# Performance work log

Hardware: AMD Instinct MI355X
Metric: run time of the kernel (lower is better)

## Reference

```python
import jax, jax.numpy as jnp
import numpy as np

E = 64      # ENTITY_EMBED_DIM
NH = 4      # ATTN_NUM_HEADS
HD = E // NH
H = 128     # RNN_HIDDEN_SIZE
LN_EPS = 1e-5

def _leaky(x):
    return jnp.where(x >= 0, x, 0.01 * x)

def setup_inputs() -> dict:
    key = jax.random.key(0)
    ks = jax.random.split(key, 20)
    def n(k, shape, s=0.1):
        return (jax.random.normal(k, shape, jnp.float32) * s)
    B, S = 128, 1024
    return {
        'obs': jax.random.normal(ks[0], (B, S, 12), jnp.float32),
        'hidden_state': jnp.zeros((1, B, H), jnp.float32),
        # missile encoder: Linear(3,32) -> LeakyReLU -> Linear(32,64)
        'me_w1': n(ks[1], (32, 3)), 'me_b1': jnp.zeros((32,), jnp.float32),
        'me_w2': n(ks[2], (64, 32)), 'me_b2': jnp.zeros((64,), jnp.float32),
        # aircraft encoder: Linear(6,32) -> LeakyReLU -> Linear(32,64)
        'ae_w1': n(ks[3], (32, 6)), 'ae_b1': jnp.zeros((32,), jnp.float32),
        'ae_w2': n(ks[4], (64, 32)), 'ae_b2': jnp.zeros((64,), jnp.float32),
        # MultiheadAttention packed in_proj (q,k,v) + out_proj
        'in_proj_w': n(ks[5], (3 * E, E)), 'in_proj_b': jnp.zeros((3 * E,), jnp.float32),
        'out_proj_w': n(ks[6], (E, E)), 'out_proj_b': jnp.zeros((E,), jnp.float32),
        # LayerNorm
        'ln_g': jnp.ones((E,), jnp.float32), 'ln_b': jnp.zeros((E,), jnp.float32),
        # GRU (r,z,n gate order, torch convention)
        'gru_w_ih': n(ks[7], (3 * H, E)), 'gru_w_hh': n(ks[8], (3 * H, H)),
        'gru_b_ih': jnp.zeros((3 * H,), jnp.float32), 'gru_b_hh': jnp.zeros((3 * H,), jnp.float32),
        # post-GRU MLP: Linear(128,128)+LeakyReLU x2
        'mlp_w0': n(ks[9], (128, 128)), 'mlp_b0': jnp.zeros((128,), jnp.float32),
        'mlp_w1': n(ks[10], (128, 128)), 'mlp_b1': jnp.zeros((128,), jnp.float32),
        # value head
        'out_w': n(ks[11], (1, 128)), 'out_b': jnp.zeros((1,), jnp.float32),
    }

def reference(obs, hidden_state, me_w1, me_b1, me_w2, me_b2, ae_w1, ae_b1, ae_w2, ae_b2,
              in_proj_w, in_proj_b, out_proj_w, out_proj_b, ln_g, ln_b,
              gru_w_ih, gru_w_hh, gru_b_ih, gru_b_hh,
              mlp_w0, mlp_b0, mlp_w1, mlp_b1, out_w, out_b):
    B, S, _ = obs.shape
    m1 = obs[..., 0:3]
    m2 = obs[..., 3:6]
    ac = obs[..., 6:12]

    def enc(x, w1, b1, w2, b2):
        return _leaky(x @ w1.T + b1) @ w2.T + b2

    m1e = enc(m1, me_w1, me_b1, me_w2, me_b2)   # [B,S,E]
    m2e = enc(m2, me_w1, me_b1, me_w2, me_b2)   # [B,S,E]
    ace = enc(ac, ae_w1, ae_b1, ae_w2, ae_b2)   # [B,S,E]

    # Cross-attention: 1 query (aircraft), 2 keys/values (missiles) per (b,s)
    wq, wk, wv = in_proj_w[:E], in_proj_w[E:2 * E], in_proj_w[2 * E:]
    bq, bk, bv = in_proj_b[:E], in_proj_b[E:2 * E], in_proj_b[2 * E:]
    q = ace @ wq.T + bq                          # [B,S,E]
    kv_in = jnp.stack([m1e, m2e], axis=2)        # [B,S,2,E]
    k = kv_in @ wk.T + bk                        # [B,S,2,E]
    v = kv_in @ wv.T + bv
    qh = q.reshape(B, S, NH, HD)
    kh = k.reshape(B, S, 2, NH, HD)
    vh = v.reshape(B, S, 2, NH, HD)
    scale = 1.0 / np.sqrt(HD)
    scores = jnp.einsum('bshd,bsnhd->bshn', qh, kh) * scale  # [B,S,NH,2]
    attn = jax.nn.softmax(scores, axis=-1)
    ctx = jnp.einsum('bshn,bsnhd->bshd', attn, vh).reshape(B, S, E)
    attn_out = ctx @ out_proj_w.T + out_proj_b

    # residual + LayerNorm
    x = attn_out + ace
    mu = jnp.mean(x, axis=-1, keepdims=True)
    var = jnp.mean((x - mu) ** 2, axis=-1, keepdims=True)
    xn = (x - mu) * jax.lax.rsqrt(var + LN_EPS) * ln_g + ln_b  # [B,S,E]

    # GRU over S (torch gate order r,z,n)
    xp = xn @ gru_w_ih.T + gru_b_ih  # [B,S,3H]

    def step(h, xt):
        hp = h @ gru_w_hh.T + gru_b_hh
        xr, xz, xg = jnp.split(xt, 3, axis=-1)
        hr, hz, hg = jnp.split(hp, 3, axis=-1)
        r = jax.nn.sigmoid(xr + hr)
        z = jax.nn.sigmoid(xz + hz)
        g = jnp.tanh(xg + r * hg)
        h_new = (1.0 - z) * g + z * h
        return h_new, h_new

    h_last, outs = jax.lax.scan(step, hidden_state[0], jnp.swapaxes(xp, 0, 1))
    gru_out = jnp.swapaxes(outs, 0, 1)  # [B,S,H]

    f = _leaky(gru_out @ mlp_w0.T + mlp_b0)
    f = _leaky(f @ mlp_w1.T + mlp_b1)
    value = f @ out_w.T + out_b  # [B,S,1]
    return value, h_last[None]
```

## Files before the change

kernel.cpp:

```cpp
#include <hip/hip_runtime.h>
#include <hip/hip_bf16.h>

#define BB 128
#define SS 1024
#define HH 128
#define G3 384
#define NT (BB * SS)

typedef __hip_bfloat16 bf16;
typedef unsigned int uint;
typedef unsigned short ushort;
typedef _Float16 f16;
typedef f16 f16x2 __attribute__((ext_vector_type(2)));
typedef f16 f16x8 __attribute__((ext_vector_type(8)));
typedef float f32x4 __attribute__((ext_vector_type(4)));

__device__ __forceinline__ float leaky(float x) { return x >= 0.f ? x : 0.01f * x; }
__device__ __forceinline__ f16x2 u2h(uint u) { return __builtin_bit_cast(f16x2, u); }
__device__ __forceinline__ uint packh2(float a, float b) {
  f16x2 h; h.x = (f16)a; h.y = (f16)b;
  return __builtin_bit_cast(uint, h);
}
__device__ __forceinline__ uint h1(float a) {
  return (uint)__builtin_bit_cast(ushort, (f16)a);
}
__device__ __forceinline__ uint bf_rne(float f) {
  uint u = __float_as_uint(f);
  return (u + 0x7FFFu + ((u >> 16) & 1u)) >> 16;
}
__device__ __forceinline__ float shflx(float v, int m) { return __shfl_xor(v, m, 64); }
__device__ __forceinline__ float dpp_xor1(float v) {
  int i = __builtin_bit_cast(int, v);
  i = __builtin_amdgcn_update_dpp(0, i, 0xB1, 0xF, 0xF, true);
  return __builtin_bit_cast(float, i);
}
__device__ __forceinline__ uint dpp_xor1_u(uint v) {
  int i = __builtin_amdgcn_update_dpp(0, (int)v, 0xB1, 0xF, 0xF, true);
  return (uint)i;
}
#define WSYNC() asm volatile("s_waitcnt lgkmcnt(0)" ::: "memory")

template <int NP>
__device__ __forceinline__ void ldrow(const float* __restrict__ p, f16x2* w) {
#pragma unroll
  for (int i = 0; i < NP; ++i) {
    f16x2 h; h.x = (f16)p[2 * i]; h.y = (f16)p[2 * i + 1];
    w[i] = h;
  }
}
__device__ __forceinline__ f16x8 ldw8(const float* __restrict__ p) {
  f16x8 v;
#pragma unroll
  for (int j = 0; j < 8; ++j) v[j] = (f16)p[j];
  return v;
}
template <int NP>
__device__ __forceinline__ float dot2l(const uint* __restrict__ x,
                                       const f16x2* __restrict__ w, float acc) {
#pragma unroll
  for (int i = 0; i < NP / 4; ++i) {
    uint4 uu = ((const uint4*)x)[i];
    acc = __builtin_amdgcn_fdot2(u2h(uu.x), w[4 * i + 0], acc, false);
    acc = __builtin_amdgcn_fdot2(u2h(uu.y), w[4 * i + 1], acc, false);
    acc = __builtin_amdgcn_fdot2(u2h(uu.z), w[4 * i + 2], acc, false);
    acc = __builtin_amdgcn_fdot2(u2h(uu.w), w[4 * i + 3], acc, false);
  }
  return acc;
}
__device__ __forceinline__ float d4(uint4 x, uint4 w, float acc) {
  acc = __builtin_amdgcn_fdot2(u2h(x.x), u2h(w.x), acc, false);
  acc = __builtin_amdgcn_fdot2(u2h(x.y), u2h(w.y), acc, false);
  acc = __builtin_amdgcn_fdot2(u2h(x.z), u2h(w.z), acc, false);
  acc = __builtin_amdgcn_fdot2(u2h(x.w), u2h(w.w), acc, false);
  return acc;
}

__global__ __launch_bounds__(256, 4) void pre_a(
    const float* __restrict__ obs, const float* __restrict__ me_w1,
    const float* __restrict__ me_b1, const float* __restrict__ me_w2,
    const float* __restrict__ me_b2, const float* __restrict__ ae_w1,
    const float* __restrict__ ae_b1, const float* __restrict__ ae_w2,
    const float* __restrict__ ae_b2, const float* __restrict__ ipw,
    const float* __restrict__ ipb, const float* __restrict__ opw,
    const float* __restrict__ opb, const float* __restrict__ lng,
    const float* __restrict__ lnb, uint* __restrict__ xnh) {
  __shared__ float ss[352];
  __shared__ __align__(16) uint4 w4[8 * 256];
  __shared__ __align__(16) uint ex[4][176];

  const int tid = threadIdx.x;
  const int wid = tid >> 6, l = tid & 63;
  if (tid < 96) ss[tid] = me_w1[tid];
  if (tid < 32) ss[96 + tid] = me_b1[tid];
  if (tid < 192) ss[128 + tid] = ae_w1[tid];
  if (tid < 32) ss[320 + tid] = ae_b1[tid];

  for (int idx = tid; idx < 2048; idx += 256) {
    const int r = idx & 255, c = idx >> 8;
    const float* src =
        (r < 192 ? ipw + (size_t)r * 64 : opw + (size_t)(r - 192) * 64) + c * 8;
    uint4 u;
    u.x = packh2(src[0], src[1]);
    u.y = packh2(src[2], src[3]);
    u.z = packh2(src[4], src[5]);
    u.w = packh2(src[6], src[7]);
    w4[(c << 8) + r] = u;
  }

  f16x2 wme2[16], wae2[16];
  ldrow<16>(me_w2 + l * 32, wme2);
  ldrow<16>(ae_w2 + l * 32, wae2);
  const float bme2 = me_b2[l], bae2 = ae_b2[l];
  const float bq = ipb[l], bk = ipb[64 + l], bv = ipb[128 + l], bop = opb[l];
  const float gl = lng[l], bl = lnb[l];
  __syncthreads();

  uint* um = ex[wid];
  uint* ua = um + 32;
  uint* e1 = um + 48;
  uint* e2 = um + 80;
  uint* ea = um + 112;
  uint* ec = um + 144;

  for (int base = blockIdx.x * 4; base < NT; base += 4096) {
    const size_t token = base + wid;
    const float4* ob4 = (const float4*)(obs + token * 12);
    float4 o0 = ob4[0], o1 = ob4[1], o2 = ob4[2];

    const int row = l & 31;
    const bool m2h = l >= 32;
    float i0 = m2h ? o0.w : o0.x, i1 = m2h ? o1.x : o0.y, i2 = m2h ? o1.y : o0.z;
    float t1 = ss[96 + row] + i0 * ss[row * 3] + i1 * ss[row * 3 + 1] + i2 * ss[row * 3 + 2];
    t1 = leaky(t1);
    float ta = ss[320 + row] + o1.z * ss[128 + row * 6] + o1.w * ss[128 + row * 6 + 1] +
               o2.x * ss[128 + row * 6 + 2] + o2.y * ss[128 + row * 6 + 3] +
               o2.z * ss[128 + row * 6 + 4] + o2.w * ss[128 + row * 6 + 5];
    ta = leaky(ta);
    float t1p = shflx(t1, 1), tap = shflx(ta, 1);
    if (!(l & 1)) {
      um[l >> 1] = packh2(t1, t1p);
      if (l < 32) ua[l >> 1] = packh2(ta, tap);
    }
    WSYNC();

    float m1e = dot2l<16>(um, wme2, bme2);
    float m2e = dot2l<16>(um + 16, wme2, bme2);
    float ace = dot2l<16>(ua, wae2, bae2);
    float m1p = shflx(m1e, 1), m2p = shflx(m2e, 1), acp = shflx(ace, 1);
    if (!(l & 1)) {
      e1[l >> 1] = packh2(m1e, m1p);
      e2[l >> 1] = packh2(m2e, m2p);
      ea[l >> 1] = packh2(ace, acp);
    }
    WSYNC();

    float q = bq, k1 = bk, k2 = bk, v1 = bv, v2 = bv;
    {
      const uint4* xe1 = (const uint4*)e1;
      const uint4* xe2 = (const uint4*)e2;
      const uint4* xea = (const uint4*)ea;
#pragma unroll
      for (int c = 0; c < 8; ++c) {
        uint4 x1 = xe1[c], x2 = xe2[c], xa = xea[c];
        uint4 uq = w4[(c << 8) + l];
        uint4 uk = w4[(c << 8) + 64 + l];
        uint4 uv = w4[(c << 8) + 128 + l];
        q = d4(xa, uq, q);
        k1 = d4(x1, uk, k1);
        k2 = d4(x2, uk, k2);
        v1 = d4(x1, uv, v1);
        v2 = d4(x2, uv, v2);
      }
    }

    float p1 = q * k1, p2 = q * k2;
    p1 += shflx(p1, 1); p2 += shflx(p2, 1);
    p1 += shflx(p1, 2); p2 += shflx(p2, 2);
    p1 += shflx(p1, 4); p2 += shflx(p2, 4);
    p1 += shflx(p1, 8); p2 += shflx(p2, 8);
    float s1 = p1 * 0.25f, s2 = p2 * 0.25f;
    float mx = fmaxf(s1, s2);
    float ev1 = __expf(s1 - mx), ev2 = __expf(s2 - mx);
    float a1 = ev1 / (ev1 + ev2);
    float ctx = a1 * v1 + (1.f - a1) * v2;
    float cxp = shflx(ctx, 1);
    if (!(l & 1)) ec[l >> 1] = packh2(ctx, cxp);
    WSYNC();

    float ao = bop;
    {
      const uint4* xec = (const uint4*)ec;
#pragma unroll
      for (int c = 0; c < 8; ++c) {
        ao = d4(xec[c], w4[(c << 8) + 192 + l], ao);
      }
    }
    float x = ao + ace;
    float s = x, s2s = x * x;
#pragma unroll
    for (int off = 32; off; off >>= 1) {
      s += shflx(s, off);
      s2s += shflx(s2s, off);
    }
    float mu = s * (1.f / 64.f);
    float var = s2s * (1.f / 64.f) - mu * mu;
    float rs = rsqrtf(var + 1e-5f);
    float xn = (x - mu) * rs * gl + bl;
    float xnp = shflx(xn, 1);
    if (!(l & 1)) xnh[token * 32 + (l >> 1)] = packh2(xn, xnp);
  }
}

__global__ __launch_bounds__(256) void pre_b(const uint* __restrict__ xnh,
                                             const float* __restrict__ wih,
                                             const float* __restrict__ bih,
                                             uint* __restrict__ xp32) {
  const int tid = threadIdx.x;
  const int l = tid & 63, wv = tid >> 6;
  const int n16 = l & 15, q = l >> 4;

  f16x8 Bf[6][2];
  float bias_l[6];
#pragma unroll
  for (int i = 0; i < 6; ++i) {
    const int n = (wv * 6 + i) * 16 + n16;
    const float* wrow = wih + (size_t)n * 64;
    Bf[i][0] = ldw8(wrow + q * 8);
    Bf[i][1] = ldw8(wrow + 32 + q * 8);
    bias_l[i] = bih[n];
  }

  for (int tile = blockIdx.x; tile < NT / 16; tile += gridDim.x) {
    const uint4* arow = (const uint4*)(xnh + (size_t)(tile * 16 + n16) * 32);
    f16x8 A0 = __builtin_bit_cast(f16x8, arow[q]);
    f16x8 A1 = __builtin_bit_cast(f16x8, arow[4 + q]);
#pragma unroll
    for (int i = 0; i < 6; ++i) {
      const int nt = wv * 6 + i;
      f32x4 acc = {0.f, 0.f, 0.f, 0.f};
      acc = __builtin_amdgcn_mfma_f32_16x16x32_f16(A0, Bf[i][0], acc, 0, 0, 0);
      acc = __builtin_amdgcn_mfma_f32_16x16x32_f16(A1, Bf[i][1], acc, 0, 0, 0);
#pragma unroll
      for (int r = 0; r < 4; ++r) {
        uint bv = bf_rne(acc[r] + bias_l[i]);
        uint pv = dpp_xor1_u(bv);
        if (!(l & 1))
          xp32[(size_t)(tile * 16 + q * 4 + r) * 192 + nt * 8 + (n16 >> 1)] =
              bv | (pv << 16);
      }
    }
  }
}

__global__ __launch_bounds__(320, 1) void gru_kernel(
    const bf16* __restrict__ xp, const float* __restrict__ hs,
    const float* __restrict__ whh, const float* __restrict__ bhh,
    ushort* __restrict__ gouth, float* __restrict__ hlast) {
  __shared__ __align__(16) uint hbuf[2][64];
  __shared__ __align__(16) uint ring[8 * 192];
  const int tid = threadIdx.x;
  const int b = blockIdx.x;
  const bool comp = tid < 256;
  const int lane = tid & 63;
  const int wv_ = tid >> 6;
  const int m = lane >> 1;
  const int par = lane & 1;
  const int j = (wv_ << 5) + m;
  const int pid = tid - 256;

  f16x2 wr[32], wz[32], wg[32];
  float br = 0.f, bz = 0.f, bg = 0.f, hprev = 0.f;
  const uint* xr32 = (const uint*)(xp + (size_t)b * SS * G3);
  uint a0 = 0, a1 = 0, a2 = 0, c0 = 0, c1 = 0, c2 = 0;
  if (comp) {
    ldrow<32>(whh + (size_t)j * HH + par * 64, wr);
    ldrow<32>(whh + (size_t)(HH + j) * HH + par * 64, wz);
    ldrow<32>(whh + (size_t)(2 * HH + j) * HH + par * 64, wg);
    br = bhh[j]; bz = bhh[HH + j]; bg = bhh[2 * HH + j];
    hprev = hs[b * HH + j];
    if (tid < 64) hbuf[0][tid] = packh2(hs[b * HH + 2 * tid], hs[b * HH + 2 * tid + 1]);
  } else {
    for (int s = 0; s < 4; ++s) {
      const uint* p = xr32 + s * 192 + pid * 3;
      uint v0 = p[0], v1 = p[1], v2 = p[2];
      uint* qq = ring + s * 192 + pid * 3;
      qq[0] = v0; qq[1] = v1; qq[2] = v2;
    }
    const uint* pa = xr32 + 4 * 192 + pid * 3;
    a0 = pa[0]; a1 = pa[1]; a2 = pa[2];
    const uint* pb = xr32 + 5 * 192 + pid * 3;
    c0 = pb[0]; c1 = pb[1]; c2 = pb[2];
  }
  __syncthreads();

  const ushort* ring_us = (const ushort*)ring;
  ushort* grow = gouth + (size_t)b * SS * HH;

#define CSTEP(TT, RD, WRI)                                                     \
  {                                                                            \
    const int slot = (TT) & 7;                                                 \
    uint bxr = ring_us[slot * 384 + j];                                        \
    uint bxz = ring_us[slot * 384 + 128 + j];                                  \
    uint bxg = ring_us[slot * 384 + 256 + j];                                  \
    const uint4* hb4 = (const uint4*)(hbuf[RD] + par * 32);                    \
    float ar = 0.f, az = 0.f, ag = 0.f;                                        \
    _Pragma("unroll") for (int i = 0; i < 8; ++i) {                            \
      uint4 hh = hb4[i];                                                       \
      f16x2 h0 = u2h(hh.x), hA = u2h(hh.y), h2 = u2h(hh.z), h3 = u2h(hh.w);    \
      ar = __builtin_amdgcn_fdot2(h0, wr[4 * i + 0], ar, false);               \
      az = __builtin_amdgcn_fdot2(h0, wz[4 * i + 0], az, false);               \
      ag = __builtin_amdgcn_fdot2(h0, wg[4 * i + 0], ag, false);               \
      ar = __builtin_amdgcn_fdot2(hA, wr[4 * i + 1], ar, false);               \
      az = __builtin_amdgcn_fdot2(hA, wz[4 * i + 1], az, false);               \
      ag = __builtin_amdgcn_fdot2(hA, wg[4 * i + 1], ag, false);               \
      ar = __builtin_amdgcn_fdot2(h2, wr[4 * i + 2], ar, false);               \
      az = __builtin_amdgcn_fdot2(h2, wz[4 * i + 2], az, false);               \
      ag = __builtin_amdgcn_fdot2(h2, wg[4 * i + 2], ag, false);               \
      ar = __builtin_amdgcn_fdot2(h3, wr[4 * i + 3], ar, false);               \
      az = __builtin_amdgcn_fdot2(h3, wz[4 * i + 3], az, false);               \
      ag = __builtin_amdgcn_fdot2(h3, wg[4 * i + 3], ag, false);               \
    }                                                                          \
    ar += dpp_xor1(ar); az += dpp_xor1(az); ag += dpp_xor1(ag);                \
    float xrf = __uint_as_float(bxr << 16);                                    \
    float xzf = __uint_as_float(bxz << 16);                                    \
    float xgf = __uint_as_float(bxg << 16);                                    \
    float r = 1.f / (1.f + __expf(-(xrf + ar + br)));                          \
    float z = 1.f / (1.f + __expf(-(xzf + az + bz)));                          \
    float gp = xgf + r * (ag + bg);                                            \
    float e = __expf(-2.f * fabsf(gp));                                        \
    float th = copysignf((1.f - e) / (1.f + e), gp);                           \
    float hn = (1.f - z) * th + z * hprev;                                     \
    hprev = hn;                                                                \
    if (!par) {                                                                \
      ((ushort*)hbuf[WRI])[j] = (ushort)h1(hn);                                \
      grow[(size_t)(TT)*HH + j] = (ushort)h1(hn);                              \
    }                                                                          \
  }

#define PSTEP(TT, R0, R1, R2)                                                  \
  {                                                                            \
    const int wrow = (TT) + 4;                                                 \
    if (wrow < SS) {                                                           \
      uint* qq = ring + (wrow & 7) * 192 + pid * 3;                            \
      qq[0] = R0; qq[1] = R1; qq[2] = R2;                                      \
      const int lrow = (TT) + 6;                                               \
      if (lrow < SS) {                                                         \
        const uint* p = xr32 + lrow * 192 + pid * 3;                           \
        R0 = p[0]; R1 = p[1]; R2 = p[2];                                       \
      }                                                                        \
    }                                                                          \
  }

  for (int t = 0; t < SS; t += 2) {
    if (comp) {
      CSTEP(t, 0, 1);
    } else {
      PSTEP(t, a0, a1, a2);
    }
    asm volatile("s_waitcnt lgkmcnt(0)\n\ts_barrier" ::: "memory");
    if (comp) {
      CSTEP(t + 1, 1, 0);
    } else {
      PSTEP(t + 1, c0, c1, c2);
    }
    asm volatile("s_waitcnt lgkmcnt(0)\n\ts_barrier" ::: "memory");
  }
#undef CSTEP
#undef PSTEP
  if (comp && !par) hlast[b * HH + j] = hprev;
}

__global__ __launch_bounds__(256) void mlp0(const uint* __restrict__ gh,
                                            const float* __restrict__ w0,
                                            const float* __restrict__ b0,
                                            uint* __restrict__ f0h32) {
  const int tid = threadIdx.x;
  const int l = tid & 63, wv = tid >> 6;
  const int n16 = l & 15, q = l >> 4;

  f16x8 Bf[2][4];
  float bias_l[2];
#pragma unroll
  for (int i = 0; i < 2; ++i) {
    const int n = (wv * 2 + i) * 16 + n16;
    const float* wrow = w0 + (size_t)n * 128;
#pragma unroll
    for (int f = 0; f < 4; ++f) Bf[i][f] = ldw8(wrow + f * 32 + q * 8);
    bias_l[i] = b0[n];
  }

  for (int tile = blockIdx.x; tile < NT / 16; tile += gridDim.x) {
    const uint4* arow = (const uint4*)(gh + (size_t)(tile * 16 + n16) * 64);
    f16x8 A[4];
#pragma unroll
    for (int f = 0; f < 4; ++f) A[f] = __builtin_bit_cast(f16x8, arow[f * 4 + q]);
#pragma unroll
    for (int i = 0; i < 2; ++i) {
      const int nt = wv * 2 + i;
      f32x4 acc = {0.f, 0.f, 0.f, 0.f};
#pragma unroll
      for (int f = 0; f < 4; ++f)
        acc = __builtin_amdgcn_mfma_f32_16x16x32_f16(A[f], Bf[i][f], acc, 0, 0, 0);
#pragma unroll
      for (int r = 0; r < 4; ++r) {
        uint hv = h1(leaky(acc[r] + bias_l[i]));
        uint pv = dpp_xor1_u(hv);
        if (!(l & 1))
          f0h32[(size_t)(tile * 16 + q * 4 + r) * 64 + nt * 8 + (n16 >> 1)] =
              hv | (pv << 16);
      }
    }
  }
}

__global__ __launch_bounds__(256) void mlp1(const uint* __restrict__ f0h,
                                            const float* __restrict__ w1,
                                            const float* __restrict__ b1,
                                            const float* __restrict__ ow,
                                            const float* __restrict__ obp,
                                            float* __restrict__ value) {
  const int tid = threadIdx.x;
  const int l = tid & 63, wv = tid >> 6;
  const int n16 = l & 15, q = l >> 4;

  f16x8 Bf[8][4];
  float bias_l[8], ow_l[8];
#pragma unroll
  for (int nt = 0; nt < 8; ++nt) {
    const int n = nt * 16 + n16;
    const float* wrow = w1 + (size_t)n * 128;
#pragma unroll
    for (int f = 0; f < 4; ++f) Bf[nt][f] = ldw8(wrow + f * 32 + q * 8);
    bias_l[nt] = b1[n];
    ow_l[nt] = ow[n];
  }
  const float obias = obp[0];

  for (int tile = blockIdx.x * 4 + wv; tile < NT / 16; tile += gridDim.x * 4) {
    const uint4* arow = (const uint4*)(f0h + (size_t)(tile * 16 + n16) * 64);
    f16x8 A[4];
#pragma unroll
    for (int f = 0; f < 4; ++f) A[f] = __builtin_bit_cast(f16x8, arow[f * 4 + q]);
    float s0 = 0.f, s1 = 0.f, s2 = 0.f, s3 = 0.f;
#pragma unroll
    for (int nt = 0; nt < 8; ++nt) {
      f32x4 acc = {0.f, 0.f, 0.f, 0.f};
#pragma unroll
      for (int f = 0; f < 4; ++f)
        acc = __builtin_amdgcn_mfma_f32_16x16x32_f16(A[f], Bf[nt][f], acc, 0, 0, 0);
      s0 += leaky(acc[0] + bias_l[nt]) * ow_l[nt];
      s1 += leaky(acc[1] + bias_l[nt]) * ow_l[nt];
      s2 += leaky(acc[2] + bias_l[nt]) * ow_l[nt];
      s3 += leaky(acc[3] + bias_l[nt]) * ow_l[nt];
    }
#pragma unroll
    for (int mask = 1; mask < 16; mask <<= 1) {
      s0 += shflx(s0, mask);
      s1 += shflx(s1, mask);
      s2 += shflx(s2, mask);
      s3 += shflx(s3, mask);
    }
    if (n16 == 0) {
      value[tile * 16 + q * 4 + 0] = s0 + obias;
      value[tile * 16 + q * 4 + 1] = s1 + obias;
      value[tile * 16 + q * 4 + 2] = s2 + obias;
      value[tile * 16 + q * 4 + 3] = s3 + obias;
    }
  }
}

__global__ void fill_sentinel(float* o, int n) {
  for (int i = blockIdx.x * blockDim.x + threadIdx.x; i < n; i += gridDim.x * blockDim.x)
    o[i] = 999.0f;
}

extern "C" void kernel_launch(void* const* d_in, const int* in_sizes, int n_in,
                              void* d_out, int out_size, void* d_ws, size_t ws_size,
                              hipStream_t stream) {
  const float* obs = (const float*)d_in[0];
  const float* hs = (const float*)d_in[1];
  const float* me_w1 = (const float*)d_in[2];
  const float* me_b1 = (const float*)d_in[3];
  const float* me_w2 = (const float*)d_in[4];
  const float* me_b2 = (const float*)d_in[5];
  const float* ae_w1 = (const float*)d_in[6];
  const float* ae_b1 = (const float*)d_in[7];
  const float* ae_w2 = (const float*)d_in[8];
  const float* ae_b2 = (const float*)d_in[9];
  const float* ipw = (const float*)d_in[10];
  const float* ipb = (const float*)d_in[11];
  const float* opw = (const float*)d_in[12];
  const float* opb = (const float*)d_in[13];
  const float* lng = (const float*)d_in[14];
  const float* lnb = (const float*)d_in[15];
  const float* wih = (const float*)d_in[16];
  const float* whh = (const float*)d_in[17];
  const float* bih = (const float*)d_in[18];
  const float* bhh = (const float*)d_in[19];
  const float* w0 = (const float*)d_in[20];
  const float* b0 = (const float*)d_in[21];
  const float* w1 = (const float*)d_in[22];
  const float* b1 = (const float*)d_in[23];
  const float* ow = (const float*)d_in[24];
  const float* ob = (const float*)d_in[25];

  const size_t regA_bytes = (size_t)NT * G3 * sizeof(bf16);
  const size_t regB_bytes = (size_t)NT * 64 * sizeof(uint);
  const size_t need = regA_bytes + regB_bytes;
  float* out = (float*)d_out;
  if (ws_size < need) {
    fill_sentinel<<<288, 256, 0, stream>>>(out, out_size);
    return;
  }

  char* ws = (char*)d_ws;
  bf16* xp = (bf16*)ws;
  uint* f0h = (uint*)ws;
  uint* xnh = (uint*)(ws + regA_bytes);
  ushort* gouth = (ushort*)(ws + regA_bytes);

  pre_a<<<1024, 256, 0, stream>>>(obs, me_w1, me_b1, me_w2, me_b2, ae_w1, ae_b1,
                                  ae_w2, ae_b2, ipw, ipb, opw, opb, lng, lnb, xnh);
  pre_b<<<1024, 256, 0, stream>>>(xnh, wih, bih, (uint*)xp);
  gru_kernel<<<BB, 320, 0, stream>>>(xp, hs, whh, bhh, gouth, out + NT);
  mlp0<<<1024, 256, 0, stream>>>((const uint*)gouth, w0, b0, f0h);
  mlp1<<<1024, 256, 0, stream>>>(f0h, w1, b1, ow, ob, out);
}
```

Baseline: 833.9 us.

## Compute GRU recurrent matvec with MFMA instead of fdot2 dot products

Replaces the per-lane fdot2 recurrent matvec in the GRU kernel with MFMA 16x16x32 f16 instructions. The hidden state is broadcast into the A operand, and each wave holds 6 column tiles of W_hh as B fragments. Only row 0 of each accumulator is used, so most of the MFMA work is wasted. The change also moves the work off the VALU and drops the DPP reduction. The risk is that the latency of 24 dependent-chain MFMAs sits on the serial critical path of each timestep.

```diff
diff --git a/kernel.cpp b/kernel.cpp
--- a/kernel.cpp
+++ b/kernel.cpp
@@ -29,11 +29,6 @@
   return (u + 0x7FFFu + ((u >> 16) & 1u)) >> 16;
 }
 __device__ __forceinline__ float shflx(float v, int m) { return __shfl_xor(v, m, 64); }
-__device__ __forceinline__ float dpp_xor1(float v) {
-  int i = __builtin_bit_cast(int, v);
-  i = __builtin_amdgcn_update_dpp(0, i, 0xB1, 0xF, 0xF, true);
-  return __builtin_bit_cast(float, i);
-}
 __device__ __forceinline__ uint dpp_xor1_u(uint v) {
   int i = __builtin_amdgcn_update_dpp(0, (int)v, 0xB1, 0xF, 0xF, true);
   return (uint)i;
@@ -256,29 +251,35 @@
     const bf16* __restrict__ xp, const float* __restrict__ hs,
     const float* __restrict__ whh, const float* __restrict__ bhh,
     ushort* __restrict__ gouth, float* __restrict__ hlast) {
-  __shared__ __align__(16) uint hbuf[2][64];
+  __shared__ __align__(16) ushort hbuf[2][HH];
   __shared__ __align__(16) uint ring[8 * 192];
   const int tid = threadIdx.x;
   const int b = blockIdx.x;
   const bool comp = tid < 256;
   const int lane = tid & 63;
-  const int wv_ = tid >> 6;
-  const int m = lane >> 1;
-  const int par = lane & 1;
-  const int j = (wv_ << 5) + m;
+  const int w = tid >> 6;
+  const int n16 = lane & 15, q = lane >> 4;
   const int pid = tid - 256;
 
-  f16x2 wr[32], wz[32], wg[32];
-  float br = 0.f, bz = 0.f, bg = 0.f, hprev = 0.f;
+  f16x8 Bf[6][4];
+  float bias_r = 0.f, bias_z = 0.f, bias_g = 0.f, hp = 0.f;
+  int idx = 0;
   const uint* xr32 = (const uint*)(xp + (size_t)b * SS * G3);
   uint a0 = 0, a1 = 0, a2 = 0, c0 = 0, c1 = 0, c2 = 0;
   if (comp) {
-    ldrow<32>(whh + (size_t)j * HH + par * 64, wr);
-    ldrow<32>(whh + (size_t)(HH + j) * HH + par * 64, wz);
-    ldrow<32>(whh + (size_t)(2 * HH + j) * HH + par * 64, wg);
-    br = bhh[j]; bz = bhh[HH + j]; bg = bhh[2 * HH + j];
-    hprev = hs[b * HH + j];
-    if (tid < 64) hbuf[0][tid] = packh2(hs[b * HH + 2 * tid], hs[b * HH + 2 * tid + 1]);
+    const int tn[6] = {2 * w, 2 * w + 1, 8 + 2 * w, 9 + 2 * w, 16 + 2 * w, 17 + 2 * w};
+#pragma unroll
+    for (int i = 0; i < 6; ++i) {
+      const float* wrow = whh + (size_t)(tn[i] * 16 + n16) * HH;
+#pragma unroll
+      for (int kt = 0; kt < 4; ++kt) Bf[i][kt] = ldw8(wrow + kt * 32 + q * 8);
+    }
+    idx = 32 * w + n16 + ((q >> 1) ? 16 : 0);
+    bias_r = bhh[idx];
+    bias_z = bhh[HH + idx];
+    bias_g = bhh[2 * HH + idx];
+    hp = hs[b * HH + idx];
+    if (tid < HH) hbuf[0][tid] = (ushort)h1(hs[b * HH + tid]);
   } else {
     for (int s = 0; s < 4; ++s) {
       const uint* p = xr32 + s * 192 + pid * 3;
@@ -295,45 +296,60 @@
 
   const ushort* ring_us = (const ushort*)ring;
   ushort* grow = gouth + (size_t)b * SS * HH;
+  const bool pub = comp && !(q & 1);
+  const int sel = q >> 1;
 
 #define CSTEP(TT, RD, WRI)                                                     \
   {                                                                            \
     const int slot = (TT) & 7;                                                 \
-    uint bxr = ring_us[slot * 384 + j];                                        \
-    uint bxz = ring_us[slot * 384 + 128 + j];                                  \
-    uint bxg = ring_us[slot * 384 + 256 + j];                                  \
-    const uint4* hb4 = (const uint4*)(hbuf[RD] + par * 32);                    \
-    float ar = 0.f, az = 0.f, ag = 0.f;                                        \
-    _Pragma("unroll") for (int i = 0; i < 8; ++i) {                            \
-      uint4 hh = hb4[i];                                                       \
-      f16x2 h0 = u2h(hh.x), hA = u2h(hh.y), h2 = u2h(hh.z), h3 = u2h(hh.w);    \
-      ar = __builtin_amdgcn_fdot2(h0, wr[4 * i + 0], ar, false);               \
-      az = __builtin_amdgcn_fdot2(h0, wz[4 * i + 0], az, false);               \
-      ag = __builtin_amdgcn_fdot2(h0, wg[4 * i + 0], ag, false);               \
-      ar = __builtin_amdgcn_fdot2(hA, wr[4 * i + 1], ar, false);               \
-      az = __builtin_amdgcn_fdot2(hA, wz[4 * i + 1], az, false);               \
-      ag = __builtin_amdgcn_fdot2(hA, wg[4 * i + 1], ag, false);               \
-      ar = __builtin_amdgcn_fdot2(h2, wr[4 * i + 2], ar, false);               \
-      az = __builtin_amdgcn_fdot2(h2, wz[4 * i + 2], az, false);               \
-      ag = __builtin_amdgcn_fdot2(h2, wg[4 * i + 2], ag, false);               \
-      ar = __builtin_amdgcn_fdot2(h3, wr[4 * i + 3], ar, false);               \
-      az = __builtin_amdgcn_fdot2(h3, wz[4 * i + 3], az, false);               \
-      ag = __builtin_amdgcn_fdot2(h3, wg[4 * i + 3], ag, false);               \
-    }                                                                          \
-    ar += dpp_xor1(ar); az += dpp_xor1(az); ag += dpp_xor1(ag);                \
-    float xrf = __uint_as_float(bxr << 16);                                    \
-    float xzf = __uint_as_float(bxz << 16);                                    \
-    float xgf = __uint_as_float(bxg << 16);                                    \
-    float r = 1.f / (1.f + __expf(-(xrf + ar + br)));                          \
-    float z = 1.f / (1.f + __expf(-(xzf + az + bz)));                          \
-    float gp = xgf + r * (ag + bg);                                            \
+    const uint4* hb = (const uint4*)hbuf[RD];                                  \
+    f16x8 A0 = __builtin_bit_cast(f16x8, hb[q]);                               \
+    f16x8 A1 = __builtin_bit_cast(f16x8, hb[4 + q]);                           \
+    f16x8 A2 = __builtin_bit_cast(f16x8, hb[8 + q]);                           \
+    f16x8 A3 = __builtin_bit_cast(f16x8, hb[12 + q]);                          \
+    f32x4 ac0 = {0.f, 0.f, 0.f, 0.f}, ac1 = ac0, ac2 = ac0, ac3 = ac0,         \
+          ac4 = ac0, ac5 = ac0;                                                \
+    ac0 = __builtin_amdgcn_mfma_f32_16x16x32_f16(A0, Bf[0][0], ac0, 0, 0, 0);  \
+    ac1 = __builtin_amdgcn_mfma_f32_16x16x32_f16(A0, Bf[1][0], ac1, 0, 0, 0);  \
+    ac2 = __builtin_amdgcn_mfma_f32_16x16x32_f16(A0, Bf[2][0], ac2, 0, 0, 0);  \
+    ac3 = __builtin_amdgcn_mfma_f32_16x16x32_f16(A0, Bf[3][0], ac3, 0, 0, 0);  \
+    ac4 = __builtin_amdgcn_mfma_f32_16x16x32_f16(A0, Bf[4][0], ac4, 0, 0, 0);  \
+    ac5 = __builtin_amdgcn_mfma_f32_16x16x32_f16(A0, Bf[5][0], ac5, 0, 0, 0);  \
+    ac0 = __builtin_amdgcn_mfma_f32_16x16x32_f16(A1, Bf[0][1], ac0, 0, 0, 0);  \
+    ac1 = __builtin_amdgcn_mfma_f32_16x16x32_f16(A1, Bf[1][1], ac1, 0, 0, 0);  \
+    ac2 = __builtin_amdgcn_mfma_f32_16x16x32_f16(A1, Bf[2][1], ac2, 0, 0, 0);  \
+    ac3 = __builtin_amdgcn_mfma_f32_16x16x32_f16(A1, Bf[3][1], ac3, 0, 0, 0);  \
+    ac4 = __builtin_amdgcn_mfma_f32_16x16x32_f16(A1, Bf[4][1], ac4, 0, 0, 0);  \
+    ac5 = __builtin_amdgcn_mfma_f32_16x16x32_f16(A1, Bf[5][1], ac5, 0, 0, 0);  \
+    ac0 = __builtin_amdgcn_mfma_f32_16x16x32_f16(A2, Bf[0][2], ac0, 0, 0, 0);  \
+    ac1 = __builtin_amdgcn_mfma_f32_16x16x32_f16(A2, Bf[1][2], ac1, 0, 0, 0);  \
+    ac2 = __builtin_amdgcn_mfma_f32_16x16x32_f16(A2, Bf[2][2], ac2, 0, 0, 0);  \
+    ac3 = __builtin_amdgcn_mfma_f32_16x16x32_f16(A2, Bf[3][2], ac3, 0, 0, 0);  \
+    ac4 = __builtin_amdgcn_mfma_f32_16x16x32_f16(A2, Bf[4][2], ac4, 0, 0, 0);  \
+    ac5 = __builtin_amdgcn_mfma_f32_16x16x32_f16(A2, Bf[5][2], ac5, 0, 0, 0);  \
+    ac0 = __builtin_amdgcn_mfma_f32_16x16x32_f16(A3, Bf[0][3], ac0, 0, 0, 0);  \
+    ac1 = __builtin_amdgcn_mfma_f32_16x16x32_f16(A3, Bf[1][3], ac1, 0, 0, 0);  \
+    ac2 = __builtin_amdgcn_mfma_f32_16x16x32_f16(A3, Bf[2][3], ac2, 0, 0, 0);  \
+    ac3 = __builtin_amdgcn_mfma_f32_16x16x32_f16(A3, Bf[3][3], ac3, 0, 0, 0);  \
+    ac4 = __builtin_amdgcn_mfma_f32_16x16x32_f16(A3, Bf[4][3], ac4, 0, 0, 0);  \
+    ac5 = __builtin_amdgcn_mfma_f32_16x16x32_f16(A3, Bf[5][3], ac5, 0, 0, 0);  \
+    float Pr = (sel ? ac1[0] : ac0[0]) + bias_r;                               \
+    float Pz = (sel ? ac3[0] : ac2[0]) + bias_z;                               \
+    float Pg = (sel ? ac5[0] : ac4[0]) + bias_g;                               \
+    uint bxr = ring_us[slot * 384 + idx];                                      \
+    uint bxz = ring_us[slot * 384 + 128 + idx];                                \
+    uint bxg = ring_us[slot * 384 + 256 + idx];                                \
+    float r = 1.f / (1.f + __expf(-(__uint_as_float(bxr << 16) + Pr)));        \
+    float z = 1.f / (1.f + __expf(-(__uint_as_float(bxz << 16) + Pz)));        \
+    float gp = __uint_as_float(bxg << 16) + r * Pg;                            \
     float e = __expf(-2.f * fabsf(gp));                                        \
     float th = copysignf((1.f - e) / (1.f + e), gp);                           \
-    float hn = (1.f - z) * th + z * hprev;                                     \
-    hprev = hn;                                                                \
-    if (!par) {                                                                \
-      ((ushort*)hbuf[WRI])[j] = (ushort)h1(hn);                                \
-      grow[(size_t)(TT)*HH + j] = (ushort)h1(hn);                              \
+    float hn = (1.f - z) * th + z * hp;                                        \
+    hp = hn;                                                                   \
+    if (pub) {                                                                 \
+      ushort hb16 = (ushort)h1(hn);                                            \
+      hbuf[WRI][idx] = hb16;                                                   \
+      grow[(size_t)(TT)*HH + idx] = hb16;                                      \
     }                                                                          \
   }
 
@@ -367,7 +383,7 @@
   }
 #undef CSTEP
 #undef PSTEP
-  if (comp && !par) hlast[b * HH + j] = hprev;
+  if (pub) hlast[b * HH + idx] = hp;
 }
 
 __global__ __launch_bounds__(256) void mlp0(const uint* __restrict__ gh,
```

Measured after the change: 787.3 us. 1.06x faster.
